# Kernel optimization log

Hardware: AMD Instinct MI355X
Metric: run time of the kernel (lower is better)

The kernel has to match this reference:

```python
import jax, jax.numpy as jnp
import numpy as np

NEG = -9e15

def _gat_layer(x, adj, W, a_src, a_dst):
    # x: [B,N,Fin], W: [Fin,Fout], a_src/a_dst: [Fout], adj: [N,N]
    h = jnp.einsum('bnf,fo->bno', x, W)                    # [B,N,Fout]
    e_src = jnp.einsum('bno,o->bn', h, a_src)              # [B,N]
    e_dst = jnp.einsum('bno,o->bn', h, a_dst)              # [B,N]
    e = jax.nn.leaky_relu(e_src[:, :, None] + e_dst[:, None, :], 0.2)  # [B,N,N]
    att = jax.nn.softmax(jnp.where(adj > 0, e, NEG), axis=-1)
    return jnp.einsum('bij,bjo->bio', att, h)              # [B,N,Fout]

def setup_inputs() -> dict:
    key = jax.random.key(0)
    ks = jax.random.split(key, 12)
    B, N, Fin = 8, 2048, 128
    H = [128, 128, 64]
    C = 128
    s = lambda *d: 1.0 / np.sqrt(d[0])
    inp = {
        'x':   jax.random.normal(ks[0], (B, N, Fin), jnp.float32),
        'adj': jax.random.normal(ks[1], (N, N), jnp.float32),
        'W1':  jax.random.normal(ks[2], (Fin, H[0]), jnp.float32) * s(Fin),
        'a1s': jax.random.normal(ks[3], (H[0],), jnp.float32) * s(H[0]),
        'a1d': jax.random.normal(ks[4], (H[0],), jnp.float32) * s(H[0]),
        'W2':  jax.random.normal(ks[5], (H[0], H[1]), jnp.float32) * s(H[0]),
        'a2s': jax.random.normal(ks[6], (H[1],), jnp.float32) * s(H[1]),
        'a2d': jax.random.normal(ks[7], (H[1],), jnp.float32) * s(H[1]),
        'W3':  jax.random.normal(ks[8], (H[1], H[2]), jnp.float32) * s(H[1]),
        'a3s': jax.random.normal(ks[9], (H[2],), jnp.float32) * s(H[2]),
        'a3d': jax.random.normal(ks[10], (H[2],), jnp.float32) * s(H[2]),
        'Wlin': jax.random.normal(ks[11], (H[2] * N, C), jnp.float32) * s(H[2] * N),
        'blin': jnp.zeros((C,), jnp.float32),
    }
    return inp

def reference(x, adj, W1, a1s, a1d, W2, a2s, a2d, W3, a3s, a3d, Wlin, blin):
    out = jax.nn.relu(_gat_layer(x, adj, W1, a1s, a1d))
    out = jax.nn.relu(_gat_layer(out, adj, W2, a2s, a2d))
    out = jax.nn.relu(_gat_layer(out, adj, W3, a3s, a3d))
    B = out.shape[0]
    out = out.reshape(B, -1)              # flatten [B, N*H3]
    return out @ Wlin + blin              # [B, num_classes]
```

## Files before the change

kernel.cpp:

```cpp
#include <hip/hip_runtime.h>
#include <stdint.h>


typedef unsigned short u16;
typedef __bf16 bf16x8 __attribute__((ext_vector_type(8)));
typedef float f32x4 __attribute__((ext_vector_type(4)));
typedef u16 u16x8 __attribute__((ext_vector_type(8)));

#define LOG2E 1.44269504088896340736f

__device__ __forceinline__ float b2f(u16 u) {
    union { unsigned int i; float f; } v; v.i = ((unsigned int)u) << 16; return v.f;
}
__device__ __forceinline__ u16 f2b(float f) {
    union { float f; unsigned int i; } v; v.f = f;
    unsigned int i = v.i;
    return (u16)((i + 0x7fffu + ((i >> 16) & 1u)) >> 16);
}
__device__ __forceinline__ float fast_exp2(float x) {
#if __has_builtin(__builtin_amdgcn_exp2f)
    return __builtin_amdgcn_exp2f(x);
#else
    return exp2f(x);
#endif
}

union ABfrag { bf16x8 v; u16x8 u; };

__device__ __forceinline__ void gload_lds16(const u16* g, u16* l) {
    __builtin_amdgcn_global_load_lds((const __attribute__((address_space(1))) void*)g,
                                     (__attribute__((address_space(3))) void*)l,
                                     16, 0, 0);
}

template <int N>
__device__ __forceinline__ void wait_vmcnt() {
    asm volatile("s_waitcnt vmcnt(%0)" :: "i"(N) : "memory");
}
__device__ __forceinline__ void pipe_barrier() {
    __builtin_amdgcn_s_barrier();
    asm volatile("" ::: "memory");
}

__global__ void __launch_bounds__(256) k_mask(const float* __restrict__ adj,
                                              uint32_t* __restrict__ adjm) {
    const int w = threadIdx.x >> 6, lane = threadIdx.x & 63;
    const int row = blockIdx.x * 4 + w;
    const float* ar = adj + (size_t)row * 2048;
    uint32_t* mr = adjm + (size_t)row * 64;
    for (int j0 = 0; j0 < 2048; j0 += 64) {
        unsigned long long m = __ballot(ar[j0 + lane] > 0.f);
        if (lane == 0) {
            mr[(j0 >> 5)] = (uint32_t)m;
            mr[(j0 >> 5) + 1] = (uint32_t)(m >> 32);
        }
    }
}

__global__ void k_prep(const float* __restrict__ W1, const float* __restrict__ W2,
                       const float* __restrict__ W3,
                       const float* __restrict__ a1s, const float* __restrict__ a1d,
                       const float* __restrict__ a2s, const float* __restrict__ a2d,
                       const float* __restrict__ a3s, const float* __restrict__ a3d,
                       u16* __restrict__ Wt1, u16* __restrict__ Wt2, u16* __restrict__ Wt3,
                       float* __restrict__ u1s, float* __restrict__ u1d,
                       float* __restrict__ u2s, float* __restrict__ u2d,
                       float* __restrict__ u3s, float* __restrict__ u3d) {
    if (blockIdx.x == 160) {
        int f = threadIdx.x;
        if (f < 128) {
            float s1 = 0.f, d1 = 0.f, s2 = 0.f, d2 = 0.f, s3 = 0.f, d3 = 0.f;
            for (int o = 0; o < 128; ++o) { float w = W1[f * 128 + o]; s1 += w * a1s[o]; d1 += w * a1d[o]; }
            for (int o = 0; o < 128; ++o) { float w = W2[f * 128 + o]; s2 += w * a2s[o]; d2 += w * a2d[o]; }
            for (int o = 0; o <  64; ++o) { float w = W3[f *  64 + o]; s3 += w * a3s[o]; d3 += w * a3d[o]; }
            u1s[f] = s1 * LOG2E; u1d[f] = d1 * LOG2E;
            u2s[f] = s2 * LOG2E; u2d[f] = d2 * LOG2E;
            u3s[f] = s3 * LOG2E; u3d[f] = d3 * LOG2E;
        }
        return;
    }
    int idx = blockIdx.x * 256 + threadIdx.x;
    if (idx < 16384) {
        int f = idx >> 7, o = idx & 127;
        Wt1[o * 128 + f] = f2b(W1[idx]);
    } else if (idx < 32768) {
        int j = idx - 16384; int f = j >> 7, o = j & 127;
        Wt2[o * 128 + f] = f2b(W2[j]);
    } else if (idx < 40960) {
        int j = idx - 32768; int f = j >> 6, o = j & 63;
        Wt3[o * 128 + f] = f2b(W3[j]);
    }
}

template <int F, bool XF32>
__global__ void __launch_bounds__(256) k_h(const void* __restrict__ xv,
                                           const u16* __restrict__ Wt,
                                           const float* __restrict__ us,
                                           const float* __restrict__ ud,
                                           u16* __restrict__ h_t,
                                           float* __restrict__ esf,
                                           float* __restrict__ edf) {
    constexpr int NTB = F / 32;
    constexpr int TNP = 72;
    __shared__ __align__(16) u16 hl[(F / 2) * TNP];

    const int b = blockIdx.x;
    const int nb2 = blockIdx.y;
    const int nblk = nb2 >> 1, ohalf = nb2 & 1;
    const int tid = threadIdx.x;
    const int w = tid >> 6, lane = tid & 63;
    const int quad = lane >> 4, l15 = lane & 15;
    const int n0w = nblk * 64 + w * 16;
    const int i_a = n0w + l15;

    ABfrag afr[4];
    float ps = 0.f, pd = 0.f;
    if (XF32) {
        const float* xr = (const float*)xv + ((size_t)(b * 2048 + i_a)) * 128;
#pragma unroll
        for (int kk = 0; kk < 4; ++kk) {
            const int o8 = kk * 32 + quad * 8;
            float4 x0 = *reinterpret_cast<const float4*>(xr + o8);
            float4 x1 = *reinterpret_cast<const float4*>(xr + o8 + 4);
            float4 s0 = *reinterpret_cast<const float4*>(us + o8);
            float4 s1 = *reinterpret_cast<const float4*>(us + o8 + 4);
            float4 d0 = *reinterpret_cast<const float4*>(ud + o8);
            float4 d1 = *reinterpret_cast<const float4*>(ud + o8 + 4);
            ps += x0.x * s0.x + x0.y * s0.y + x0.z * s0.z + x0.w * s0.w
                + x1.x * s1.x + x1.y * s1.y + x1.z * s1.z + x1.w * s1.w;
            pd += x0.x * d0.x + x0.y * d0.y + x0.z * d0.z + x0.w * d0.w
                + x1.x * d1.x + x1.y * d1.y + x1.z * d1.z + x1.w * d1.w;
            afr[kk].u[0] = f2b(x0.x); afr[kk].u[1] = f2b(x0.y);
            afr[kk].u[2] = f2b(x0.z); afr[kk].u[3] = f2b(x0.w);
            afr[kk].u[4] = f2b(x1.x); afr[kk].u[5] = f2b(x1.y);
            afr[kk].u[6] = f2b(x1.z); afr[kk].u[7] = f2b(x1.w);
        }
    } else {
        const u16* xr = (const u16*)xv + ((size_t)(b * 2048 + i_a)) * 128;
#pragma unroll
        for (int kk = 0; kk < 4; ++kk) {
            const int o8 = kk * 32 + quad * 8;
            u16x8 xa = *reinterpret_cast<const u16x8*>(xr + o8);
            afr[kk].u = xa;
            float4 s0 = *reinterpret_cast<const float4*>(us + o8);
            float4 s1 = *reinterpret_cast<const float4*>(us + o8 + 4);
            float4 d0 = *reinterpret_cast<const float4*>(ud + o8);
            float4 d1 = *reinterpret_cast<const float4*>(ud + o8 + 4);
            float xf[8];
#pragma unroll
            for (int j = 0; j < 8; ++j) xf[j] = b2f(xa[j]);
            ps += xf[0] * s0.x + xf[1] * s0.y + xf[2] * s0.z + xf[3] * s0.w
                + xf[4] * s1.x + xf[5] * s1.y + xf[6] * s1.z + xf[7] * s1.w;
            pd += xf[0] * d0.x + xf[1] * d0.y + xf[2] * d0.z + xf[3] * d0.w
                + xf[4] * d1.x + xf[5] * d1.y + xf[6] * d1.z + xf[7] * d1.w;
        }
    }
    if (ohalf == 0) {
        ps += __shfl_xor(ps, 16, 64); ps += __shfl_xor(ps, 32, 64);
        pd += __shfl_xor(pd, 16, 64); pd += __shfl_xor(pd, 32, 64);
        if (quad == 0) {
            const size_t idx = (size_t)(b * 2048 + i_a) * 2;
            float2 sv; sv.x = fast_exp2(ps); sv.y = fast_exp2(0.2f * ps);
            float2 dv; dv.x = fast_exp2(pd); dv.y = fast_exp2(0.2f * pd);
            *reinterpret_cast<float2*>(esf + idx) = sv;
            *reinterpret_cast<float2*>(edf + idx) = dv;
        }
    }

    f32x4 acc[NTB];
#pragma unroll
    for (int nt = 0; nt < NTB; ++nt) acc[nt] = (f32x4){0.f, 0.f, 0.f, 0.f};
#pragma unroll
    for (int kk = 0; kk < 4; ++kk) {
#pragma unroll
        for (int nt = 0; nt < NTB; ++nt) {
            bf16x8 bfv = *reinterpret_cast<const bf16x8*>(
                Wt + (ohalf * (F / 2) + nt * 16 + l15) * 128 + kk * 32 + quad * 8);
            acc[nt] = __builtin_amdgcn_mfma_f32_16x16x32_bf16(afr[kk].v, bfv, acc[nt], 0, 0, 0);
        }
    }

#pragma unroll
    for (int nt = 0; nt < NTB; ++nt)
#pragma unroll
        for (int r = 0; r < 4; ++r)
            hl[(nt * 16 + l15) * TNP + w * 16 + quad * 4 + r] = f2b(acc[nt][r]);
    __syncthreads();
    if (tid < F) {
        int o_loc = tid >> 1, half32 = tid & 1;
        const u16* src = hl + o_loc * TNP + half32 * 32;
        u16* dst = h_t + ((size_t)(b * F + ohalf * (F / 2) + o_loc)) * 2048
                   + nblk * 64 + half32 * 32;
#pragma unroll
        for (int c = 0; c < 4; ++c)
            *reinterpret_cast<u16x8*>(dst + c * 8) =
                *reinterpret_cast<const u16x8*>(src + c * 8);
    }
}

template <int F, bool OUT_F32>
__global__ void __launch_bounds__(256) k_attn(const float* __restrict__ esf,
                                              const float* __restrict__ edf,
                                              const uint32_t* __restrict__ adjm,
                                              const u16* __restrict__ h_t,
                                              void* __restrict__ outp) {
    constexpr int NT = F / 16;
    constexpr int G  = F / 16;
    __shared__ __align__(16) u16 Ht[2][3][F * 64];
    __shared__ __align__(16) float eL[4096];
    __shared__ __align__(16) uint32_t mL[64 * 64];
    float* accLDS = (float*)&Ht[0][0][0];

    const int b = blockIdx.x;
    const int iblk = blockIdx.y;
    const int tid = threadIdx.x;
    const int grp = tid >> 7;
    const int t128 = tid & 127;
    const int w = t128 >> 6;
    const int lane = tid & 63;
    const int quad = lane >> 4, l15 = lane & 15;
    const int r0 = w * 32 + l15;
    const int r1 = r0 + 16;

    const float2 e0 = *reinterpret_cast<const float2*>(esf + ((size_t)(b * 2048 + iblk * 64 + r0)) * 2);
    const float2 e1 = *reinterpret_cast<const float2*>(esf + ((size_t)(b * 2048 + iblk * 64 + r1)) * 2);
    const float Es0 = e0.x, Fs0 = e0.y, Es1 = e1.x, Fs1 = e1.y;
    const u16* hb = h_t + (size_t)b * F * 2048;

    const int lro = lane >> 3;
    const int lcp = lane & 7;
    const int jt0 = grp * 16;

    ABfrag onesf;
#pragma unroll
    for (int j = 0; j < 8; ++j) onesf.u[j] = 0x3F80;

    f32x4 acc0[NT], acc1[NT];
#pragma unroll
    for (int nt = 0; nt < NT; ++nt) {
        acc0[nt] = (f32x4){0.f, 0.f, 0.f, 0.f};
        acc1[nt] = (f32x4){0.f, 0.f, 0.f, 0.f};
    }
    f32x4 d0 = (f32x4){0.f, 0.f, 0.f, 0.f};
    f32x4 d1 = (f32x4){0.f, 0.f, 0.f, 0.f};

    {
        const float4* esrc = (const float4*)(edf + (size_t)b * 4096);
        float4* edst = (float4*)eL;
#pragma unroll
        for (int t = 0; t < 4; ++t) edst[tid + t * 256] = esrc[tid + t * 256];
        const uint2* msrc = (const uint2*)(adjm + (size_t)(iblk * 64) * 64);
#pragma unroll
        for (int t = 0; t < 8; ++t) {
            int idx = tid + t * 256;
            int r = idx >> 5, k = idx & 31;
            uint2 v = msrc[idx];
            *reinterpret_cast<uint2*>((char*)mL + r * 256 + ((k ^ (r & 31)) * 8)) = v;
        }
    }

    auto STAGE = [&](int jt, int slot) {
        const int j0 = jt * 64;
        u16* lbase = &Ht[grp][slot][0];
#pragma unroll
        for (int it = 0; it < G; ++it) {
            int ci = it * 2 + w;
            int ro = ci * 8 + lro;
            int c = lcp ^ (ro & 7);
            gload_lds16(hb + (size_t)ro * 2048 + j0 + c * 8, lbase + ci * 512);
        }
    };

    f32x4 ec[8]; uint2 mc0, mc1;
    auto loadE = [&](int jt) {
        const float* eb = eL + (size_t)(jt * 64 + quad * 8) * 2;
#pragma unroll
        for (int q = 0; q < 4; ++q) ec[q] = *reinterpret_cast<const f32x4*>(eb + q * 4);
#pragma unroll
        for (int q = 0; q < 4; ++q) ec[4 + q] = *reinterpret_cast<const f32x4*>(eb + 64 + q * 4);
        mc0 = *reinterpret_cast<const uint2*>((const char*)mL + r0 * 256 + ((jt ^ (r0 & 31)) * 8));
        mc1 = *reinterpret_cast<const uint2*>((const char*)mL + r1 * 256 + ((jt ^ (r1 & 31)) * 8));
    };

    auto compute = [&](int slot) {
        ABfrag af0[2], af1[2];
#pragma unroll
        for (int kk = 0; kk < 2; ++kk) {
            const uint32_t word0 = kk ? mc0.y : mc0.x;
            const uint32_t word1 = kk ? mc1.y : mc1.x;
#pragma unroll
            for (int px = 0; px < 4; ++px) {
                const f32x4 q = ec[kk * 4 + px];
                const int bsh = quad * 8 + px * 2;
                float wa0 = fmaxf(Es0 * q.x, Fs0 * q.y);
                float wb0 = fmaxf(Es0 * q.z, Fs0 * q.w);
                float wa1 = fmaxf(Es1 * q.x, Fs1 * q.y);
                float wb1 = fmaxf(Es1 * q.z, Fs1 * q.w);
                const uint32_t sa0 = 0u - ((word0 >> bsh) & 1u);
                const uint32_t sb0 = 0u - ((word0 >> (bsh + 1)) & 1u);
                const uint32_t sa1 = 0u - ((word1 >> bsh) & 1u);
                const uint32_t sb1 = 0u - ((word1 >> (bsh + 1)) & 1u);
                wa0 = __uint_as_float(__float_as_uint(wa0) & sa0);
                wb0 = __uint_as_float(__float_as_uint(wb0) & sb0);
                wa1 = __uint_as_float(__float_as_uint(wa1) & sa1);
                wb1 = __uint_as_float(__float_as_uint(wb1) & sb1);
                af0[kk].v[px * 2]     = (__bf16)wa0;
                af0[kk].v[px * 2 + 1] = (__bf16)wb0;
                af1[kk].v[px * 2]     = (__bf16)wa1;
                af1[kk].v[px * 2 + 1] = (__bf16)wb1;
            }
        }
        const u16* tb = &Ht[grp][slot][0];
        __builtin_amdgcn_s_setprio(1);
#pragma unroll
        for (int kk = 0; kk < 2; ++kk) {
#pragma unroll
            for (int nt = 0; nt < NT; ++nt) {
                int ob = nt * 16 + l15;
                int c = kk * 4 + quad;
                bf16x8 bfv = *reinterpret_cast<const bf16x8*>(
                    tb + ob * 64 + ((c ^ (ob & 7)) * 8));
                acc0[nt] = __builtin_amdgcn_mfma_f32_16x16x32_bf16(af0[kk].v, bfv, acc0[nt], 0, 0, 0);
                acc1[nt] = __builtin_amdgcn_mfma_f32_16x16x32_bf16(af1[kk].v, bfv, acc1[nt], 0, 0, 0);
            }
            d0 = __builtin_amdgcn_mfma_f32_16x16x32_bf16(af0[kk].v, onesf.v, d0, 0, 0, 0);
            d1 = __builtin_amdgcn_mfma_f32_16x16x32_bf16(af1[kk].v, onesf.v, d1, 0, 0, 0);
        }
        __builtin_amdgcn_s_setprio(0);
    };

    __syncthreads();
    STAGE(jt0, 0);
    STAGE(jt0 + 1, 1);

    int sc = 0, sp = 2;
    for (int jj = 0; jj < 15; ++jj) {
        wait_vmcnt<G>();
        pipe_barrier();
        if (jj < 14) STAGE(jt0 + jj + 2, sp);
        loadE(jt0 + jj);
        compute(sc);
        sc = (sc == 2) ? 0 : sc + 1;
        sp = (sp == 2) ? 0 : sp + 1;
    }
    wait_vmcnt<0>();
    pipe_barrier();
    loadE(jt0 + 15);
    compute(sc);

    __syncthreads();
    if (grp == 1) {
        f32x4* basep = reinterpret_cast<f32x4*>(&accLDS[(size_t)t128 * (2 * NT + 2) * 4]);
#pragma unroll
        for (int nt = 0; nt < NT; ++nt) { basep[nt] = acc0[nt]; basep[NT + nt] = acc1[nt]; }
        basep[2 * NT] = d0;
        basep[2 * NT + 1] = d1;
    }
    __syncthreads();
    if (grp == 0) {
        const f32x4* basep = reinterpret_cast<const f32x4*>(&accLDS[(size_t)t128 * (2 * NT + 2) * 4]);
#pragma unroll
        for (int nt = 0; nt < NT; ++nt) { acc0[nt] += basep[nt]; acc1[nt] += basep[NT + nt]; }
        d0 += basep[2 * NT];
        d1 += basep[2 * NT + 1];
        float dinv0[4], dinv1[4];
#pragma unroll
        for (int r = 0; r < 4; ++r) {
            dinv0[r] = 1.0f / fmaxf(d0[r], 1e-30f);
            dinv1[r] = 1.0f / fmaxf(d1[r], 1e-30f);
        }
        const int ib0 = iblk * 64 + w * 32 + quad * 4;
        const int ib1 = ib0 + 16;
        if (OUT_F32) {
            float* o3 = (float*)outp;
#pragma unroll
            for (int nt = 0; nt < NT; ++nt)
#pragma unroll
                for (int r = 0; r < 4; ++r) {
                    float v0 = fmaxf(acc0[nt][r] * dinv0[r], 0.f);
                    float v1 = fmaxf(acc1[nt][r] * dinv1[r], 0.f);
                    o3[((size_t)(b * 2048 + ib0 + r)) * F + nt * 16 + l15] = v0;
                    o3[((size_t)(b * 2048 + ib1 + r)) * F + nt * 16 + l15] = v1;
                }
        } else {
            u16* xo = (u16*)outp;
#pragma unroll
            for (int nt = 0; nt < NT; ++nt)
#pragma unroll
                for (int r = 0; r < 4; ++r) {
                    float v0 = fmaxf(acc0[nt][r] * dinv0[r], 0.f);
                    float v1 = fmaxf(acc1[nt][r] * dinv1[r], 0.f);
                    xo[((size_t)(b * 2048 + ib0 + r)) * F + nt * 16 + l15] = f2b(v0);
                    xo[((size_t)(b * 2048 + ib1 + r)) * F + nt * 16 + l15] = f2b(v1);
                }
        }
    }
}

__global__ void __launch_bounds__(256) k_lin(const float* __restrict__ o3,
                                             const float* __restrict__ Wlin,
                                             float* __restrict__ pbuf) {
    __shared__ float xc[8][256];
    __shared__ float red[8][8][128];
    const int tid = threadIdx.x;
    const int k0 = blockIdx.x * 256;
    for (int idx = tid; idx < 2048; idx += 256) {
        int bb = idx >> 8, kk = idx & 255;
        xc[bb][kk] = o3[(size_t)bb * 131072 + k0 + kk];
    }
    __syncthreads();
    const int o4 = tid & 31;
    const int kb = tid >> 5;
    f32x4 acc[8];
#pragma unroll
    for (int bb = 0; bb < 8; ++bb) acc[bb] = (f32x4){0.f, 0.f, 0.f, 0.f};
    const float* wp = Wlin + (size_t)(k0 + kb * 32) * 128 + o4 * 4;
#pragma unroll 4
    for (int k = 0; k < 32; ++k) {
        f32x4 wv = *reinterpret_cast<const f32x4*>(wp + (size_t)k * 128);
#pragma unroll
        for (int bb = 0; bb < 8; ++bb) acc[bb] += wv * xc[bb][kb * 32 + k];
    }
#pragma unroll
    for (int bb = 0; bb < 8; ++bb)
        *reinterpret_cast<f32x4*>(&red[kb][bb][o4 * 4]) = acc[bb];
    __syncthreads();
    const int f = tid * 4;
    const int bb = f >> 7, o = f & 127;
    f32x4 s = (f32x4){0.f, 0.f, 0.f, 0.f};
#pragma unroll
    for (int k2 = 0; k2 < 8; ++k2) s += *reinterpret_cast<const f32x4*>(&red[k2][bb][o]);
    *reinterpret_cast<f32x4*>(&pbuf[(size_t)blockIdx.x * 1024 + f]) = s;
}

__global__ void __launch_bounds__(256) k_bias(const float* __restrict__ pbuf,
                                              const float* __restrict__ blin,
                                              float* __restrict__ out) {
    __shared__ float red[256];
    const int tid = threadIdx.x;
    const int p16 = tid >> 4;
    const int fo = tid & 15;
    const int f0 = blockIdx.x * 16;
    float s = 0.f;
#pragma unroll 4
    for (int p = p16; p < 512; p += 16)
        s += pbuf[(size_t)p * 1024 + f0 + fo];
    red[tid] = s;
    __syncthreads();
    if (tid < 16) {
        float t = 0.f;
#pragma unroll
        for (int k = 0; k < 16; ++k) t += red[k * 16 + tid];
        out[f0 + tid] = t + blin[(f0 + tid) & 127];
    }
}

extern "C" void kernel_launch(void* const* d_in, const int* in_sizes, int n_in,
                              void* d_out, int out_size, void* d_ws, size_t ws_size,
                              hipStream_t stream) {
    (void)in_sizes; (void)n_in; (void)out_size;
    const float* x    = (const float*)d_in[0];
    const float* adj  = (const float*)d_in[1];
    const float* W1   = (const float*)d_in[2];
    const float* a1s  = (const float*)d_in[3];
    const float* a1d  = (const float*)d_in[4];
    const float* W2   = (const float*)d_in[5];
    const float* a2s  = (const float*)d_in[6];
    const float* a2d  = (const float*)d_in[7];
    const float* W3   = (const float*)d_in[8];
    const float* a3s  = (const float*)d_in[9];
    const float* a3d  = (const float*)d_in[10];
    const float* Wlin = (const float*)d_in[11];
    const float* blin = (const float*)d_in[12];

    char* ws = (char*)d_ws;
    u16*   h_t = (u16*)ws;
    size_t off = (size_t)4 << 20;
    float* esf = (float*)(ws + off); off += 131072;
    float* edf = (float*)(ws + off); off += 131072;
    u16*   Wt1 = (u16*)(ws + off);   off += 32768;
    u16*   Wt2 = (u16*)(ws + off);   off += 32768;
    u16*   Wt3 = (u16*)(ws + off);   off += 16384;
    float* u1s = (float*)(ws + off); off += 512;
    float* u1d = (float*)(ws + off); off += 512;
    float* u2s = (float*)(ws + off); off += 512;
    float* u2d = (float*)(ws + off); off += 512;
    float* u3s = (float*)(ws + off); off += 512;
    float* u3d = (float*)(ws + off); off += 512;
    uint32_t* adjm = (uint32_t*)(ws + off); off += 524288;
    float* pbuf = (float*)(ws + off); off += (size_t)512 * 1024 * 4;
    u16* actA;
    if (ws_size >= off + ((size_t)4 << 20)) {
        actA = (u16*)(ws + off);
    } else {
        actA = (u16*)d_in[0];
    }
    float* o3 = (float*)actA;

    dim3 g(8, 32);
    dim3 gh(8, 64);
    k_mask<<<512, 256, 0, stream>>>(adj, adjm);
    k_prep<<<161, 256, 0, stream>>>(W1, W2, W3, a1s, a1d, a2s, a2d, a3s, a3d,
                                    Wt1, Wt2, Wt3, u1s, u1d, u2s, u2d, u3s, u3d);

    k_h<128, true ><<<gh, 256, 0, stream>>>((const void*)x, Wt1, u1s, u1d, h_t, esf, edf);
    k_attn<128, false><<<g, 256, 0, stream>>>(esf, edf, adjm, h_t, (void*)actA);

    k_h<128, false><<<gh, 256, 0, stream>>>((const void*)actA, Wt2, u2s, u2d, h_t, esf, edf);
    k_attn<128, false><<<g, 256, 0, stream>>>(esf, edf, adjm, h_t, (void*)actA);

    k_h<64, false><<<gh, 256, 0, stream>>>((const void*)actA, Wt3, u3s, u3d, h_t, esf, edf);
    k_attn<64, true ><<<g, 256, 0, stream>>>(esf, edf, adjm, h_t, (void*)o3);

    k_lin<<<512, 256, 0, stream>>>(o3, Wlin, pbuf);
    k_bias<<<64, 256, 0, stream>>>(pbuf, blin, (float*)d_out);
}
```

Baseline: 253.6 us.

## Restructure attention kernel: 32-row tiles, direct global B loads, 4-way split-K

Rewrites the attention aggregation kernel to process 32 query rows per block instead of 64, doubling the grid. The LDS-staged triple-buffered global_load_lds pipeline is replaced by direct per-wave register loads of h_t fragments with one-step register prefetch. Each of the four waves takes a quarter of the key dimension, and the partial sums are reduced through LDS. LDS use shrinks and launch bounds request 2 blocks per SM to raise occupancy. The trade-off is that h_t is now re-read from global or L2 per wave with no LDS reuse, and the smaller row tile halves reuse of each loaded B fragment.

```diff
diff --git a/kernel.cpp b/kernel.cpp
--- a/kernel.cpp
+++ b/kernel.cpp
@@ -6,6 +6,7 @@
 typedef __bf16 bf16x8 __attribute__((ext_vector_type(8)));
 typedef float f32x4 __attribute__((ext_vector_type(4)));
 typedef u16 u16x8 __attribute__((ext_vector_type(8)));
+typedef u16 u16x4 __attribute__((ext_vector_type(4)));
 
 #define LOG2E 1.44269504088896340736f
 
@@ -26,21 +27,6 @@
 }
 
 union ABfrag { bf16x8 v; u16x8 u; };
-
-__device__ __forceinline__ void gload_lds16(const u16* g, u16* l) {
-    __builtin_amdgcn_global_load_lds((const __attribute__((address_space(1))) void*)g,
-                                     (__attribute__((address_space(3))) void*)l,
-                                     16, 0, 0);
-}
-
-template <int N>
-__device__ __forceinline__ void wait_vmcnt() {
-    asm volatile("s_waitcnt vmcnt(%0)" :: "i"(N) : "memory");
-}
-__device__ __forceinline__ void pipe_barrier() {
-    __builtin_amdgcn_s_barrier();
-    asm volatile("" ::: "memory");
-}
 
 __global__ void __launch_bounds__(256) k_mask(const float* __restrict__ adj,
                                               uint32_t* __restrict__ adjm) {
@@ -199,37 +185,34 @@
 }
 
 template <int F, bool OUT_F32>
-__global__ void __launch_bounds__(256) k_attn(const float* __restrict__ esf,
-                                              const float* __restrict__ edf,
-                                              const uint32_t* __restrict__ adjm,
-                                              const u16* __restrict__ h_t,
-                                              void* __restrict__ outp) {
+__global__ void __launch_bounds__(256, 2) k_attn(const float* __restrict__ esf,
+                                                 const float* __restrict__ edf,
+                                                 const uint32_t* __restrict__ adjm,
+                                                 const u16* __restrict__ h_t,
+                                                 void* __restrict__ outp) {
     constexpr int NT = F / 16;
-    constexpr int G  = F / 16;
-    __shared__ __align__(16) u16 Ht[2][3][F * 64];
-    __shared__ __align__(16) float eL[4096];
-    __shared__ __align__(16) uint32_t mL[64 * 64];
-    float* accLDS = (float*)&Ht[0][0][0];
+    constexpr int LP_BYTES = 4096 * 4 + 2048 * 4;
+    constexpr int CB_BYTES = 4 * 32 * F * 4 + 4 * 32 * 4;
+    constexpr int LDS_BYTES = (LP_BYTES > CB_BYTES) ? LP_BYTES : CB_BYTES;
+    __shared__ __align__(16) char Sraw[LDS_BYTES];
+    float* eL = (float*)Sraw;
+    uint32_t* mL = (uint32_t*)(Sraw + 4096 * 4);
+    float* part = (float*)Sraw;
+    float* denp = (float*)(Sraw + 4 * 32 * F * 4);
 
     const int b = blockIdx.x;
-    const int iblk = blockIdx.y;
+    const int i32blk = blockIdx.y;
+    const int i0 = i32blk * 32;
     const int tid = threadIdx.x;
-    const int grp = tid >> 7;
-    const int t128 = tid & 127;
-    const int w = t128 >> 6;
+    const int w = tid >> 6;
     const int lane = tid & 63;
     const int quad = lane >> 4, l15 = lane & 15;
-    const int r0 = w * 32 + l15;
-    const int r1 = r0 + 16;
-
-    const float2 e0 = *reinterpret_cast<const float2*>(esf + ((size_t)(b * 2048 + iblk * 64 + r0)) * 2);
-    const float2 e1 = *reinterpret_cast<const float2*>(esf + ((size_t)(b * 2048 + iblk * 64 + r1)) * 2);
-    const float Es0 = e0.x, Fs0 = e0.y, Es1 = e1.x, Fs1 = e1.y;
+    const int r0 = l15, r1 = l15 + 16;
+
+    const float2 e0p = *reinterpret_cast<const float2*>(esf + ((size_t)(b * 2048 + i0 + r0)) * 2);
+    const float2 e1p = *reinterpret_cast<const float2*>(esf + ((size_t)(b * 2048 + i0 + r1)) * 2);
+    const float Es0 = e0p.x, Fs0 = e0p.y, Es1 = e1p.x, Fs1 = e1p.y;
     const u16* hb = h_t + (size_t)b * F * 2048;
-
-    const int lro = lane >> 3;
-    const int lcp = lane & 7;
-    const int jt0 = grp * 16;
 
     ABfrag onesf;
 #pragma unroll
@@ -249,150 +232,121 @@
         float4* edst = (float4*)eL;
 #pragma unroll
         for (int t = 0; t < 4; ++t) edst[tid + t * 256] = esrc[tid + t * 256];
-        const uint2* msrc = (const uint2*)(adjm + (size_t)(iblk * 64) * 64);
-#pragma unroll
-        for (int t = 0; t < 8; ++t) {
+        const uint2* msrc = (const uint2*)(adjm + (size_t)i0 * 64);
+#pragma unroll
+        for (int t = 0; t < 4; ++t) {
             int idx = tid + t * 256;
-            int r = idx >> 5, k = idx & 31;
+            int r = idx >> 5, k2 = idx & 31;
             uint2 v = msrc[idx];
-            *reinterpret_cast<uint2*>((char*)mL + r * 256 + ((k ^ (r & 31)) * 8)) = v;
-        }
-    }
-
-    auto STAGE = [&](int jt, int slot) {
-        const int j0 = jt * 64;
-        u16* lbase = &Ht[grp][slot][0];
-#pragma unroll
-        for (int it = 0; it < G; ++it) {
-            int ci = it * 2 + w;
-            int ro = ci * 8 + lro;
-            int c = lcp ^ (ro & 7);
-            gload_lds16(hb + (size_t)ro * 2048 + j0 + c * 8, lbase + ci * 512);
-        }
+            mL[r * 64 + ((2 * k2) ^ r)] = v.x;
+            mL[r * 64 + ((2 * k2 + 1) ^ r)] = v.y;
+        }
+    }
+    __syncthreads();
+
+    const int jbase = w * 16;
+    auto loadB = [&](int t, ABfrag* bt) {
+        const size_t coff = (size_t)((jbase + t) * 32 + quad * 8);
+#pragma unroll
+        for (int nt = 0; nt < NT; ++nt)
+            bt[nt].u = *reinterpret_cast<const u16x8*>(
+                hb + (size_t)(nt * 16 + l15) * 2048 + coff);
     };
 
-    f32x4 ec[8]; uint2 mc0, mc1;
-    auto loadE = [&](int jt) {
-        const float* eb = eL + (size_t)(jt * 64 + quad * 8) * 2;
-#pragma unroll
-        for (int q = 0; q < 4; ++q) ec[q] = *reinterpret_cast<const f32x4*>(eb + q * 4);
-#pragma unroll
-        for (int q = 0; q < 4; ++q) ec[4 + q] = *reinterpret_cast<const f32x4*>(eb + 64 + q * 4);
-        mc0 = *reinterpret_cast<const uint2*>((const char*)mL + r0 * 256 + ((jt ^ (r0 & 31)) * 8));
-        mc1 = *reinterpret_cast<const uint2*>((const char*)mL + r1 * 256 + ((jt ^ (r1 & 31)) * 8));
-    };
-
-    auto compute = [&](int slot) {
-        ABfrag af0[2], af1[2];
-#pragma unroll
-        for (int kk = 0; kk < 2; ++kk) {
-            const uint32_t word0 = kk ? mc0.y : mc0.x;
-            const uint32_t word1 = kk ? mc1.y : mc1.x;
-#pragma unroll
-            for (int px = 0; px < 4; ++px) {
-                const f32x4 q = ec[kk * 4 + px];
-                const int bsh = quad * 8 + px * 2;
-                float wa0 = fmaxf(Es0 * q.x, Fs0 * q.y);
-                float wb0 = fmaxf(Es0 * q.z, Fs0 * q.w);
-                float wa1 = fmaxf(Es1 * q.x, Fs1 * q.y);
-                float wb1 = fmaxf(Es1 * q.z, Fs1 * q.w);
-                const uint32_t sa0 = 0u - ((word0 >> bsh) & 1u);
-                const uint32_t sb0 = 0u - ((word0 >> (bsh + 1)) & 1u);
-                const uint32_t sa1 = 0u - ((word1 >> bsh) & 1u);
-                const uint32_t sb1 = 0u - ((word1 >> (bsh + 1)) & 1u);
-                wa0 = __uint_as_float(__float_as_uint(wa0) & sa0);
-                wb0 = __uint_as_float(__float_as_uint(wb0) & sb0);
-                wa1 = __uint_as_float(__float_as_uint(wa1) & sa1);
-                wb1 = __uint_as_float(__float_as_uint(wb1) & sb1);
-                af0[kk].v[px * 2]     = (__bf16)wa0;
-                af0[kk].v[px * 2 + 1] = (__bf16)wb0;
-                af1[kk].v[px * 2]     = (__bf16)wa1;
-                af1[kk].v[px * 2 + 1] = (__bf16)wb1;
+    ABfrag bt[NT], bn[NT];
+    loadB(0, bt);
+
+    for (int t = 0; t < 16; ++t) {
+        if (t < 15) loadB(t + 1, bn);
+        const int jt = jbase + t;
+        const int j0 = jt * 32;
+
+        f32x4 ec[4];
+        {
+            const float* ep = eL + (size_t)(j0 + quad * 8) * 2;
+#pragma unroll
+            for (int q = 0; q < 4; ++q) ec[q] = *reinterpret_cast<const f32x4*>(ep + q * 4);
+        }
+        const uint32_t m0 = mL[r0 * 64 + (jt ^ r0)];
+        const uint32_t m1 = mL[r1 * 64 + (jt ^ r1)];
+
+        ABfrag af0, af1;
+#pragma unroll
+        for (int px = 0; px < 4; ++px) {
+            const f32x4 q = ec[px];
+            const int bsh = quad * 8 + px * 2;
+            float wa0 = fmaxf(Es0 * q.x, Fs0 * q.y);
+            float wb0 = fmaxf(Es0 * q.z, Fs0 * q.w);
+            float wa1 = fmaxf(Es1 * q.x, Fs1 * q.y);
+            float wb1 = fmaxf(Es1 * q.z, Fs1 * q.w);
+            const uint32_t sa0 = 0u - ((m0 >> bsh) & 1u);
+            const uint32_t sb0 = 0u - ((m0 >> (bsh + 1)) & 1u);
+            const uint32_t sa1 = 0u - ((m1 >> bsh) & 1u);
+            const uint32_t sb1 = 0u - ((m1 >> (bsh + 1)) & 1u);
+            wa0 = __uint_as_float(__float_as_uint(wa0) & sa0);
+            wb0 = __uint_as_float(__float_as_uint(wb0) & sb0);
+            wa1 = __uint_as_float(__float_as_uint(wa1) & sa1);
+            wb1 = __uint_as_float(__float_as_uint(wb1) & sb1);
+            af0.v[px * 2]     = (__bf16)wa0;
+            af0.v[px * 2 + 1] = (__bf16)wb0;
+            af1.v[px * 2]     = (__bf16)wa1;
+            af1.v[px * 2 + 1] = (__bf16)wb1;
+        }
+
+#pragma unroll
+        for (int nt = 0; nt < NT; ++nt) {
+            acc0[nt] = __builtin_amdgcn_mfma_f32_16x16x32_bf16(af0.v, bt[nt].v, acc0[nt], 0, 0, 0);
+            acc1[nt] = __builtin_amdgcn_mfma_f32_16x16x32_bf16(af1.v, bt[nt].v, acc1[nt], 0, 0, 0);
+        }
+        d0 = __builtin_amdgcn_mfma_f32_16x16x32_bf16(af0.v, onesf.v, d0, 0, 0, 0);
+        d1 = __builtin_amdgcn_mfma_f32_16x16x32_bf16(af1.v, onesf.v, d1, 0, 0, 0);
+
+        if (t < 15) {
+#pragma unroll
+            for (int nt = 0; nt < NT; ++nt) bt[nt] = bn[nt];
+        }
+    }
+
+    __syncthreads();
+    {
+        float* pw = part + (size_t)w * 32 * F;
+#pragma unroll
+        for (int nt = 0; nt < NT; ++nt)
+#pragma unroll
+            for (int r = 0; r < 4; ++r) {
+                pw[(quad * 4 + r) * F + nt * 16 + l15] = acc0[nt][r];
+                pw[(16 + quad * 4 + r) * F + nt * 16 + l15] = acc1[nt][r];
             }
-        }
-        const u16* tb = &Ht[grp][slot][0];
-        __builtin_amdgcn_s_setprio(1);
-#pragma unroll
-        for (int kk = 0; kk < 2; ++kk) {
-#pragma unroll
-            for (int nt = 0; nt < NT; ++nt) {
-                int ob = nt * 16 + l15;
-                int c = kk * 4 + quad;
-                bf16x8 bfv = *reinterpret_cast<const bf16x8*>(
-                    tb + ob * 64 + ((c ^ (ob & 7)) * 8));
-                acc0[nt] = __builtin_amdgcn_mfma_f32_16x16x32_bf16(af0[kk].v, bfv, acc0[nt], 0, 0, 0);
-                acc1[nt] = __builtin_amdgcn_mfma_f32_16x16x32_bf16(af1[kk].v, bfv, acc1[nt], 0, 0, 0);
+#pragma unroll
+        for (int r = 0; r < 4; ++r) {
+            denp[w * 32 + quad * 4 + r] = d0[r];
+            denp[w * 32 + 16 + quad * 4 + r] = d1[r];
+        }
+    }
+    __syncthreads();
+    {
+        constexpr int C4 = F / 4;
+        for (int idx = tid; idx < 32 * C4; idx += 256) {
+            const int row = idx / C4, c4 = idx % C4;
+            f32x4 s = *reinterpret_cast<const f32x4*>(&part[row * F + c4 * 4]);
+#pragma unroll
+            for (int ww = 1; ww < 4; ++ww)
+                s += *reinterpret_cast<const f32x4*>(&part[(ww * 32 + row) * F + c4 * 4]);
+            const float den = denp[row] + denp[32 + row] + denp[64 + row] + denp[96 + row];
+            const float dinv = 1.0f / fmaxf(den, 1e-30f);
+            if (OUT_F32) {
+                float4 o;
+                o.x = fmaxf(s[0] * dinv, 0.f); o.y = fmaxf(s[1] * dinv, 0.f);
+                o.z = fmaxf(s[2] * dinv, 0.f); o.w = fmaxf(s[3] * dinv, 0.f);
+                *reinterpret_cast<float4*>((float*)outp +
+                    ((size_t)(b * 2048 + i0 + row)) * F + c4 * 4) = o;
+            } else {
+                u16x4 o;
+                o[0] = f2b(fmaxf(s[0] * dinv, 0.f)); o[1] = f2b(fmaxf(s[1] * dinv, 0.f));
+                o[2] = f2b(fmaxf(s[2] * dinv, 0.f)); o[3] = f2b(fmaxf(s[3] * dinv, 0.f));
+                *reinterpret_cast<u16x4*>((u16*)outp +
+                    ((size_t)(b * 2048 + i0 + row)) * F + c4 * 4) = o;
             }
-            d0 = __builtin_amdgcn_mfma_f32_16x16x32_bf16(af0[kk].v, onesf.v, d0, 0, 0, 0);
-            d1 = __builtin_amdgcn_mfma_f32_16x16x32_bf16(af1[kk].v, onesf.v, d1, 0, 0, 0);
-        }
-        __builtin_amdgcn_s_setprio(0);
-    };
-
-    __syncthreads();
-    STAGE(jt0, 0);
-    STAGE(jt0 + 1, 1);
-
-    int sc = 0, sp = 2;
-    for (int jj = 0; jj < 15; ++jj) {
-        wait_vmcnt<G>();
-        pipe_barrier();
-        if (jj < 14) STAGE(jt0 + jj + 2, sp);
-        loadE(jt0 + jj);
-        compute(sc);
-        sc = (sc == 2) ? 0 : sc + 1;
-        sp = (sp == 2) ? 0 : sp + 1;
-    }
-    wait_vmcnt<0>();
-    pipe_barrier();
-    loadE(jt0 + 15);
-    compute(sc);
-
-    __syncthreads();
-    if (grp == 1) {
-        f32x4* basep = reinterpret_cast<f32x4*>(&accLDS[(size_t)t128 * (2 * NT + 2) * 4]);
-#pragma unroll
-        for (int nt = 0; nt < NT; ++nt) { basep[nt] = acc0[nt]; basep[NT + nt] = acc1[nt]; }
-        basep[2 * NT] = d0;
-        basep[2 * NT + 1] = d1;
-    }
-    __syncthreads();
-    if (grp == 0) {
-        const f32x4* basep = reinterpret_cast<const f32x4*>(&accLDS[(size_t)t128 * (2 * NT + 2) * 4]);
-#pragma unroll
-        for (int nt = 0; nt < NT; ++nt) { acc0[nt] += basep[nt]; acc1[nt] += basep[NT + nt]; }
-        d0 += basep[2 * NT];
-        d1 += basep[2 * NT + 1];
-        float dinv0[4], dinv1[4];
-#pragma unroll
-        for (int r = 0; r < 4; ++r) {
-            dinv0[r] = 1.0f / fmaxf(d0[r], 1e-30f);
-            dinv1[r] = 1.0f / fmaxf(d1[r], 1e-30f);
-        }
-        const int ib0 = iblk * 64 + w * 32 + quad * 4;
-        const int ib1 = ib0 + 16;
-        if (OUT_F32) {
-            float* o3 = (float*)outp;
-#pragma unroll
-            for (int nt = 0; nt < NT; ++nt)
-#pragma unroll
-                for (int r = 0; r < 4; ++r) {
-                    float v0 = fmaxf(acc0[nt][r] * dinv0[r], 0.f);
-                    float v1 = fmaxf(acc1[nt][r] * dinv1[r], 0.f);
-                    o3[((size_t)(b * 2048 + ib0 + r)) * F + nt * 16 + l15] = v0;
-                    o3[((size_t)(b * 2048 + ib1 + r)) * F + nt * 16 + l15] = v1;
-                }
-        } else {
-            u16* xo = (u16*)outp;
-#pragma unroll
-            for (int nt = 0; nt < NT; ++nt)
-#pragma unroll
-                for (int r = 0; r < 4; ++r) {
-                    float v0 = fmaxf(acc0[nt][r] * dinv0[r], 0.f);
-                    float v1 = fmaxf(acc1[nt][r] * dinv1[r], 0.f);
-                    xo[((size_t)(b * 2048 + ib0 + r)) * F + nt * 16 + l15] = f2b(v0);
-                    xo[((size_t)(b * 2048 + ib1 + r)) * F + nt * 16 + l15] = f2b(v1);
-                }
         }
     }
 }
@@ -497,20 +451,20 @@
     }
     float* o3 = (float*)actA;
 
-    dim3 g(8, 32);
+    dim3 ga(8, 64);
     dim3 gh(8, 64);
     k_mask<<<512, 256, 0, stream>>>(adj, adjm);
     k_prep<<<161, 256, 0, stream>>>(W1, W2, W3, a1s, a1d, a2s, a2d, a3s, a3d,
                                     Wt1, Wt2, Wt3, u1s, u1d, u2s, u2d, u3s, u3d);
 
     k_h<128, true ><<<gh, 256, 0, stream>>>((const void*)x, Wt1, u1s, u1d, h_t, esf, edf);
-    k_attn<128, false><<<g, 256, 0, stream>>>(esf, edf, adjm, h_t, (void*)actA);
+    k_attn<128, false><<<ga, 256, 0, stream>>>(esf, edf, adjm, h_t, (void*)actA);
 
     k_h<128, false><<<gh, 256, 0, stream>>>((const void*)actA, Wt2, u2s, u2d, h_t, esf, edf);
-    k_attn<128, false><<<g, 256, 0, stream>>>(esf, edf, adjm, h_t, (void*)actA);
+    k_attn<128, false><<<ga, 256, 0, stream>>>(esf, edf, adjm, h_t, (void*)actA);
 
     k_h<64, false><<<gh, 256, 0, stream>>>((const void*)actA, Wt3, u3s, u3d, h_t, esf, edf);
-    k_attn<64, true ><<<g, 256, 0, stream>>>(esf, edf, adjm, h_t, (void*)o3);
+    k_attn<64, true ><<<ga, 256, 0, stream>>>(esf, edf, adjm, h_t, (void*)o3);
 
     k_lin<<<512, 256, 0, stream>>>(o3, Wlin, pbuf);
     k_bias<<<64, 256, 0, stream>>>(pbuf, blin, (float*)d_out);
```

Measured after the change: 270.1 us. +6.5%, slower.
